# Kernel optimization log

Measured on AMD Instinct MI355X. Metric: run time of the kernel, lower is better.

The kernel has to match this reference:

```python
import jax, jax.numpy as jnp
import numpy as np

TAU = 100.0
DT = 20.0
ALPHA = DT / TAU  # 0.2, fixed buffer (train_alpha=False)


def setup_inputs() -> dict:
    key = jax.random.key(0)
    ks = jax.random.split(key, 12)
    T, B, I, H = 64, 32, 128, 256

    def lin(kw, out_f, in_f):
        bound = 1.0 / np.sqrt(in_f)
        kw1, kw2 = jax.random.split(kw)
        w = jax.random.uniform(kw1, (out_f, in_f), jnp.float32, -bound, bound)
        b = jax.random.uniform(kw2, (out_f,), jnp.float32, -bound, bound)
        return w, b

    w_i2h, b_i2h = lin(ks[0], H, I)
    w_h2h, b_h2h = lin(ks[1], H, H)
    w_i2c, b_i2c = lin(ks[2], H, I)
    w_c2c, b_c2c = lin(ks[3], H, H)
    w_c2t, b_c2t = lin(ks[4], H * H, H)
    x = jax.random.normal(ks[5], (T, B, I), jnp.float32)
    return {
        "input": x,
        "w_i2h": w_i2h, "b_i2h": b_i2h,
        "w_h2h": w_h2h, "b_h2h": b_h2h,
        "w_i2c": w_i2c, "b_i2c": b_i2c,
        "w_c2c": w_c2c, "b_c2c": b_c2c,
        "w_c2t": w_c2t, "b_c2t": b_c2t,
        "num_steps": 1,
    }


def reference(input, w_i2h, b_i2h, w_h2h, b_h2h, w_i2c, b_i2c,
              w_c2c, b_c2c, w_c2t, b_c2t, num_steps):
    H = w_i2h.shape[0]
    B = input.shape[1]
    a = jnp.float32(ALPHA)

    def recurrence(x, hidden, context):
        input_proj = x @ w_i2h.T + b_i2h                      # [B,H]
        tm = (context @ w_c2t.T + b_c2t).reshape(B, H, H)     # per-sample hypernet matrix
        transformed = jnp.einsum('bij,bj->bi', tm, input_proj)
        h_new = jax.nn.relu(context + transformed + hidden @ w_h2h.T + b_h2h)
        hidden = hidden * (1 - a) + h_new * a
        context_new = jax.nn.relu(context @ w_c2c.T + b_c2c + x @ w_i2c.T + b_i2c)
        context = context * (1 - a) + context_new * a
        hidden = transformed  # NOTE: faithful to source, overwrites leaky update
        return hidden, context

    def step(carry, x):
        hidden, context = carry
        for _ in range(num_steps):
            hidden, context = recurrence(x, hidden, context)
        return (hidden, context), hidden

    h0 = jnp.zeros((B, H), input.dtype)
    c0 = jnp.zeros((B, H), input.dtype)
    (hidden, context), output = jax.lax.scan(step, (h0, c0), input)
    return output, hidden, context
```

## Files before the change

kernel.cpp:

```cpp
#include <hip/hip_runtime.h>

#define TT 64
#define BB 32
#define II 128
#define HH 256
#define MM (TT*BB)

typedef __bf16  bf16x8  __attribute__((ext_vector_type(8)));
typedef float   f32x16  __attribute__((ext_vector_type(16)));
typedef _Float16 half2v __attribute__((ext_vector_type(2)));

__device__ __forceinline__ float bf2f(unsigned short u) {
    union { unsigned int i; float f; } v; v.i = ((unsigned int)u) << 16; return v.f;
}
__device__ __forceinline__ unsigned short f2bf(float f) {
    union { float f; unsigned int i; } v; v.f = f;
    unsigned int r = v.i + 0x7fffu + ((v.i >> 16) & 1u);
    return (unsigned short)(r >> 16);
}

struct F8 { float v[8]; };
__device__ __forceinline__ F8 load8(const void* base, int idx, int isf32) {
    F8 r;
    if (isf32) {
        const float4* p = (const float4*)((const float*)base + idx);
        float4 a = p[0], b = p[1];
        r.v[0]=a.x; r.v[1]=a.y; r.v[2]=a.z; r.v[3]=a.w;
        r.v[4]=b.x; r.v[5]=b.y; r.v[6]=b.z; r.v[7]=b.w;
    } else {
        uint4 u = *(const uint4*)((const unsigned short*)base + idx);
        const unsigned short* p = (const unsigned short*)&u;
#pragma unroll
        for (int j = 0; j < 8; ++j) r.v[j] = bf2f(p[j]);
    }
    return r;
}
__device__ __forceinline__ float load1(const void* base, int idx, int isf32) {
    return isf32 ? ((const float*)base)[idx]
                 : bf2f(((const unsigned short*)base)[idx]);
}

__device__ __forceinline__ float fdot2f(half2v a, half2v b, float c) {
#if __has_builtin(__builtin_amdgcn_fdot2)
    return __builtin_amdgcn_fdot2(a, b, c, false);
#else
    return c + (float)a.x*(float)b.x + (float)a.y*(float)b.y;
#endif
}

__global__ __launch_bounds__(256) void k0_sniff(
    const unsigned short* __restrict__ x, int* __restrict__ flag)
{
    __shared__ int cnt;
    if (threadIdx.x == 0) cnt = 0;
    __syncthreads();
    int c = 0;
    for (int i = threadIdx.x; i < 8192; i += 256) {
        unsigned int e = (x[i] >> 7) & 0xFFu;
        if (e >= 0xC0u) ++c;
    }
    atomicAdd(&cnt, c);
    __syncthreads();
    if (threadIdx.x == 0) flag[0] = (cnt > 16) ? 1 : 0;
}

__global__ __launch_bounds__(256) void k1_proj(
    const void* __restrict__ x,
    const void* __restrict__ w_i2h,
    const void* __restrict__ b_i2h,
    const void* __restrict__ w_i2c,
    const void* __restrict__ b_i2c,
    const int* __restrict__ flagp,
    unsigned short* __restrict__ ip,
    float* __restrict__ cin)
{
    const int isf32 = *flagp;
    const int tid = threadIdx.x;
    const int h = tid;
    const int mbase = blockIdx.x * 32;
    __shared__ __align__(16) _Float16 xs[32][II];

    half2v w1[II/2], w2[II/2];
#pragma unroll
    for (int c8 = 0; c8 < II/8; ++c8) {
        F8 f1 = load8(w_i2h, h*II + c8*8, isf32);
        F8 f2 = load8(w_i2c, h*II + c8*8, isf32);
#pragma unroll
        for (int j = 0; j < 4; ++j) {
            half2v a; a.x = (_Float16)f1.v[2*j]; a.y = (_Float16)f1.v[2*j+1];
            half2v b; b.x = (_Float16)f2.v[2*j]; b.y = (_Float16)f2.v[2*j+1];
            w1[c8*4 + j] = a;
            w2[c8*4 + j] = b;
        }
    }
    const float bb1 = load1(b_i2h, h, isf32);
    const float bb2 = load1(b_i2c, h, isf32);

    for (int u = tid; u < 32*II; u += 256)
        xs[u >> 7][u & (II-1)] = (_Float16)load1(x, (mbase + (u >> 7))*II + (u & (II-1)), isf32);
    __syncthreads();

    for (int mm = 0; mm < 32; ++mm) {
        const half2v* xv = (const half2v*)xs[mm];
        float a0=0,a1=0,a2=0,a3=0, c0=0,c1=0,c2=0,c3=0;
#pragma unroll
        for (int r = 0; r < II/2; r += 4) {
            half2v x0 = xv[r], x1 = xv[r+1], x2 = xv[r+2], x3 = xv[r+3];
            a0 = fdot2f(w1[r],   x0, a0);
            a1 = fdot2f(w1[r+1], x1, a1);
            a2 = fdot2f(w1[r+2], x2, a2);
            a3 = fdot2f(w1[r+3], x3, a3);
            c0 = fdot2f(w2[r],   x0, c0);
            c1 = fdot2f(w2[r+1], x1, c1);
            c2 = fdot2f(w2[r+2], x2, c2);
            c3 = fdot2f(w2[r+3], x3, c3);
        }
        ip[(mbase+mm)*HH + h]  = f2bf(((a0+a1)+(a2+a3)) + bb1);
        cin[(mbase+mm)*HH + h] = ((c0+c1)+(c2+c3)) + bb2;
    }
}

__global__ __launch_bounds__(256) void k2_ctx(
    const void* __restrict__ w_c2c,
    const void* __restrict__ b_c2c,
    const float* __restrict__ cin,
    const int* __restrict__ ns_ptr,
    const int* __restrict__ flagp,
    unsigned short* __restrict__ ctx_hist,
    void* __restrict__ out_base)
{
    const int isf32 = *flagp;
    const int b = blockIdx.x;
    const int h = threadIdx.x;
    const int ns = max(1, *ns_ptr);

    __shared__ __align__(16) _Float16 cs[2][HH];

    half2v w[HH/2];
#pragma unroll
    for (int c8 = 0; c8 < HH/8; ++c8) {
        F8 f = load8(w_c2c, h*HH + c8*8, isf32);
#pragma unroll
        for (int j = 0; j < 4; ++j) {
            half2v hv;
            hv.x = (_Float16)f.v[2*j];
            hv.y = (_Float16)f.v[2*j+1];
            w[c8*4 + j] = hv;
        }
    }
    const float bcc = load1(b_c2c, h, isf32);
    float ctxv = 0.0f;
    cs[0][h] = (_Float16)0.0f;
    __syncthreads();
    int cur = 0;

    for (int t = 0; t < TT; ++t) {
        const float cinv = cin[(t*BB + b)*HH + h];
        for (int s = 0; s < ns; ++s) {
            if (s == ns-1) ctx_hist[(t*BB + b)*HH + h] = f2bf(ctxv);
            float p0=0,p1=0,p2=0,p3=0;
            const float4* cp4 = (const float4*)cs[cur];
#pragma unroll
            for (int r4 = 0; r4 < HH/8; ++r4) {
                float4 blob = cp4[r4];
                const half2v* c2 = (const half2v*)&blob;
                p0 = fdot2f(w[r4*4+0], c2[0], p0);
                p1 = fdot2f(w[r4*4+1], c2[1], p1);
                p2 = fdot2f(w[r4*4+2], c2[2], p2);
                p3 = fdot2f(w[r4*4+3], c2[3], p3);
            }
            float cnew = fmaxf(((p0+p1)+(p2+p3)) + bcc + cinv, 0.0f);
            ctxv = 0.8f*ctxv + 0.2f*cnew;
            cs[cur^1][h] = (_Float16)ctxv;
            cur ^= 1;
            __syncthreads();
        }
    }
    const int cofs = MM*HH + BB*HH + b*HH + h;
    if (isf32) ((float*)out_base)[cofs] = ctxv;
    else       ((unsigned short*)out_base)[cofs] = f2bf(ctxv);
}

__global__ __launch_bounds__(512, 2) void k3_main(
    const unsigned short* __restrict__ ctx_hist,
    const void* __restrict__ wc,
    const void* __restrict__ bc,
    const unsigned short* __restrict__ ip,
    const int* __restrict__ flagp,
    void* __restrict__ out)
{
    extern __shared__ __align__(16) unsigned char lds[];
    unsigned short* Bs = (unsigned short*)lds;
    unsigned short* As = (unsigned short*)(lds + 131072);
    float*          TMf = (float*)(lds + 131072);

    const int isf32 = *flagp;
    const int tid  = threadIdx.x;
    const int lane = tid & 63;
    const int wave = tid >> 6;
    const int i    = blockIdx.x;
    const int mh   = wave & 3;
    const int jh   = wave >> 2;
    const int l31  = lane & 31;
    const int lhi  = lane >> 5;

    const int eml = tid >> 4;
    const int ecs = tid & 15;

    float bcp[16];
    {
        F8 f0 = load8(bc, i*HH + ecs*16,     isf32);
        F8 f1 = load8(bc, i*HH + ecs*16 + 8, isf32);
#pragma unroll
        for (int j = 0; j < 8; ++j) { bcp[j] = f0.v[j]; bcp[8+j] = f1.v[j]; }
    }

#pragma unroll
    for (int p = 0; p < 16; ++p) {
        int u = tid + p*512;
        int row = u >> 5, cu = u & 31;
        F8 f = load8(wc, (i*HH + row)*HH + cu*8, isf32);
        unsigned short tmp[8];
#pragma unroll
        for (int j = 0; j < 8; ++j) tmp[j] = f2bf(f.v[j]);
        *(uint4*)(Bs + row*256 + ((cu ^ (row & 7)) << 3)) = *(const uint4*)tmp;
    }

    for (int mc = 0; mc < 8; ++mc) {
        const int m0 = mc * 256;

        f32x16 acc[2][4];
#pragma unroll
        for (int a = 0; a < 2; ++a)
#pragma unroll
            for (int n = 0; n < 4; ++n)
#pragma unroll
                for (int r = 0; r < 16; ++r) acc[a][n][r] = 0.0f;

#pragma unroll
        for (int kc = 0; kc < 4; ++kc) {
            const int k0 = kc * 64;
#pragma unroll
            for (int p = 0; p < 4; ++p) {
                int u = tid + p*512;
                int row = u >> 3, cu = u & 7;
                uint4 v = *(const uint4*)(ctx_hist + (m0 + row)*HH + k0 + cu*8);
                *(uint4*)(As + row*64 + ((cu ^ (row & 7)) << 3)) = v;
            }
            __syncthreads();
#pragma unroll
            for (int ks = 0; ks < 4; ++ks) {
                const int cA = ks*2 + lhi;
                const int ra0 = mh*64 + l31;
                const int ra1 = ra0 + 32;
                bf16x8 a0 = *(const bf16x8*)(As + ra0*64 + ((cA ^ (ra0 & 7)) << 3));
                bf16x8 a1 = *(const bf16x8*)(As + ra1*64 + ((cA ^ (ra1 & 7)) << 3));
                const int cB = kc*8 + ks*2 + lhi;
                const int rb0 = jh*128 +       l31;
                const int rb1 = jh*128 + 32  + l31;
                const int rb2 = jh*128 + 64  + l31;
                const int rb3 = jh*128 + 96  + l31;
                bf16x8 b0 = *(const bf16x8*)(Bs + rb0*256 + ((cB ^ (rb0 & 7)) << 3));
                bf16x8 b1 = *(const bf16x8*)(Bs + rb1*256 + ((cB ^ (rb1 & 7)) << 3));
                bf16x8 b2 = *(const bf16x8*)(Bs + rb2*256 + ((cB ^ (rb2 & 7)) << 3));
                bf16x8 b3 = *(const bf16x8*)(Bs + rb3*256 + ((cB ^ (rb3 & 7)) << 3));
                acc[0][0] = __builtin_amdgcn_mfma_f32_32x32x16_bf16(a0, b0, acc[0][0], 0, 0, 0);
                acc[0][1] = __builtin_amdgcn_mfma_f32_32x32x16_bf16(a0, b1, acc[0][1], 0, 0, 0);
                acc[0][2] = __builtin_amdgcn_mfma_f32_32x32x16_bf16(a0, b2, acc[0][2], 0, 0, 0);
                acc[0][3] = __builtin_amdgcn_mfma_f32_32x32x16_bf16(a0, b3, acc[0][3], 0, 0, 0);
                acc[1][0] = __builtin_amdgcn_mfma_f32_32x32x16_bf16(a1, b0, acc[1][0], 0, 0, 0);
                acc[1][1] = __builtin_amdgcn_mfma_f32_32x32x16_bf16(a1, b1, acc[1][1], 0, 0, 0);
                acc[1][2] = __builtin_amdgcn_mfma_f32_32x32x16_bf16(a1, b2, acc[1][2], 0, 0, 0);
                acc[1][3] = __builtin_amdgcn_mfma_f32_32x32x16_bf16(a1, b3, acc[1][3], 0, 0, 0);
            }
            __syncthreads();
        }

#pragma unroll
        for (int ch = 0; ch < 8; ++ch) {
            if (mh == (ch >> 1)) {
                const int a = ch & 1;
#pragma unroll
                for (int n = 0; n < 4; ++n) {
                    const int j  = jh*128 + n*32 + l31;
                    const int ju = j >> 2, jo = j & 3;
#pragma unroll
                    for (int r = 0; r < 16; ++r) {
                        const int row16 = (r & 3) + 8*(r >> 2) + 4*lhi;
                        TMf[row16*256 + ((ju ^ (row16 & 7)) << 2) + jo] = acc[a][n][r];
                    }
                }
            }
            __syncthreads();
            {
                const int g = m0 + ch*32 + eml;
                float ipf[16];
                {
                    uint4 u0 = *(const uint4*)(ip + g*HH + ecs*16);
                    uint4 u1 = *(const uint4*)(ip + g*HH + ecs*16 + 8);
                    const unsigned short* p0 = (const unsigned short*)&u0;
                    const unsigned short* p1 = (const unsigned short*)&u1;
#pragma unroll
                    for (int j = 0; j < 8; ++j) { ipf[j] = bf2f(p0[j]); ipf[8+j] = bf2f(p1[j]); }
                }
                const float4* TM4 = (const float4*)TMf;
                float s = 0.0f;
#pragma unroll
                for (int u = 0; u < 4; ++u) {
                    float4 t = TM4[eml*64 + ((ecs*4 + u) ^ (eml & 7))];
                    s = fmaf(t.x + bcp[u*4+0], ipf[u*4+0], s);
                    s = fmaf(t.y + bcp[u*4+1], ipf[u*4+1], s);
                    s = fmaf(t.z + bcp[u*4+2], ipf[u*4+2], s);
                    s = fmaf(t.w + bcp[u*4+3], ipf[u*4+3], s);
                }
                s += __shfl_xor(s, 1);
                s += __shfl_xor(s, 2);
                s += __shfl_xor(s, 4);
                s += __shfl_xor(s, 8);
                if (ecs == 0) {
                    if (isf32) {
                        float* o = (float*)out;
                        o[g*HH + i] = s;
                        if (g >= MM - BB) o[MM*HH + (g - (MM-BB))*HH + i] = s;
                    } else {
                        unsigned short* o = (unsigned short*)out;
                        const unsigned short v = f2bf(s);
                        o[g*HH + i] = v;
                        if (g >= MM - BB) o[MM*HH + (g - (MM-BB))*HH + i] = v;
                    }
                }
            }
            __syncthreads();
        }
    }
}

extern "C" void kernel_launch(void* const* d_in, const int* in_sizes, int n_in,
                              void* d_out, int out_size, void* d_ws, size_t ws_size,
                              hipStream_t stream) {
    const void* x     = d_in[0];
    const void* w_i2h = d_in[1];
    const void* b_i2h = d_in[2];
    const void* w_i2c = d_in[5];
    const void* b_i2c = d_in[6];
    const void* w_c2c = d_in[7];
    const void* b_c2c = d_in[8];
    const void* w_c2t = d_in[9];
    const void* b_c2t = d_in[10];
    const int* ns     = (const int*)d_in[11];

    unsigned short* ip  = (unsigned short*)d_ws;
    unsigned short* ch  = (unsigned short*)((char*)d_ws + (size_t)MM*HH*2);
    float* cin          = (float*)((char*)d_ws + (size_t)MM*HH*4);
    int* flag           = (int*)((char*)d_ws + (size_t)MM*HH*8);

    static bool attr_done = false;
    (void)hipFuncSetAttribute((const void*)k3_main,
                              hipFuncAttributeMaxDynamicSharedMemorySize, 163840);
    (void)attr_done;

    k0_sniff<<<1, 256, 0, stream>>>((const unsigned short*)x, flag);
    k1_proj<<<64, 256, 0, stream>>>(x, w_i2h, b_i2h, w_i2c, b_i2c, flag, ip, cin);
    k2_ctx<<<BB, 256, 0, stream>>>(w_c2c, b_c2c, cin, ns, flag, ch, d_out);
    k3_main<<<256, 512, 163840, stream>>>(ch, w_c2t, b_c2t, ip, flag, d_out);
}
```

Measured before the change: 341.5 us.

## Prefetch A tiles into registers and reduce epilogue directly from MFMA accumulators

The main hypernet GEMM kernel now prefetches the next context-history tile into registers while the current tile is consumed by MFMAs. The epilogue drops the staged LDS round-trip of the transformed matrix and instead dots accumulators with the input projection in registers, reducing with shuffles. Results go to a transposed fp32 scratch buffer that a new transpose kernel writes out coalesced. This adds an extra launch and scratch traffic, and lowers launch bounds to one block per CU.

Result: slower. 405.6 us (+18.8%).

```diff
diff --git a/kernel.cpp b/kernel.cpp
--- a/kernel.cpp
+++ b/kernel.cpp
@@ -181,18 +181,18 @@
     else       ((unsigned short*)out_base)[cofs] = f2bf(ctxv);
 }
 
-__global__ __launch_bounds__(512, 2) void k3_main(
+__global__ __launch_bounds__(512, 1) void k3_main(
     const unsigned short* __restrict__ ctx_hist,
     const void* __restrict__ wc,
     const void* __restrict__ bc,
     const unsigned short* __restrict__ ip,
     const int* __restrict__ flagp,
-    void* __restrict__ out)
+    float* __restrict__ outT)
 {
     extern __shared__ __align__(16) unsigned char lds[];
     unsigned short* Bs = (unsigned short*)lds;
     unsigned short* As = (unsigned short*)(lds + 131072);
-    float*          TMf = (float*)(lds + 131072);
+    float*          part = (float*)(lds + 131072);
 
     const int isf32 = *flagp;
     const int tid  = threadIdx.x;
@@ -204,16 +204,10 @@
     const int l31  = lane & 31;
     const int lhi  = lane >> 5;
 
-    const int eml = tid >> 4;
-    const int ecs = tid & 15;
-
-    float bcp[16];
-    {
-        F8 f0 = load8(bc, i*HH + ecs*16,     isf32);
-        F8 f1 = load8(bc, i*HH + ecs*16 + 8, isf32);
-#pragma unroll
-        for (int j = 0; j < 8; ++j) { bcp[j] = f0.v[j]; bcp[8+j] = f1.v[j]; }
-    }
+    float bcv[4];
+#pragma unroll
+    for (int n = 0; n < 4; ++n)
+        bcv[n] = load1(bc, i*HH + jh*128 + n*32 + l31, isf32);
 
 #pragma unroll
     for (int p = 0; p < 16; ++p) {
@@ -226,6 +220,14 @@
         *(uint4*)(Bs + row*256 + ((cu ^ (row & 7)) << 3)) = *(const uint4*)tmp;
     }
 
+    uint4 areg[4];
+#pragma unroll
+    for (int p = 0; p < 4; ++p) {
+        int u = tid + p*512;
+        int row = u >> 3, cu = u & 7;
+        areg[p] = *(const uint4*)(ctx_hist + row*HH + cu*8);
+    }
+
     for (int mc = 0; mc < 8; ++mc) {
         const int m0 = mc * 256;
 
@@ -239,15 +241,27 @@
 
 #pragma unroll
         for (int kc = 0; kc < 4; ++kc) {
-            const int k0 = kc * 64;
+            __syncthreads();
 #pragma unroll
             for (int p = 0; p < 4; ++p) {
                 int u = tid + p*512;
                 int row = u >> 3, cu = u & 7;
-                uint4 v = *(const uint4*)(ctx_hist + (m0 + row)*HH + k0 + cu*8);
-                *(uint4*)(As + row*64 + ((cu ^ (row & 7)) << 3)) = v;
+                *(uint4*)(As + row*64 + ((cu ^ (row & 7)) << 3)) = areg[p];
             }
             __syncthreads();
+            {
+                int nmc = mc, nkc = kc + 1;
+                if (nkc == 4) { nkc = 0; nmc = mc + 1; }
+                if (nmc < 8) {
+                    const unsigned short* src = ctx_hist + (nmc*256)*HH + nkc*64;
+#pragma unroll
+                    for (int p = 0; p < 4; ++p) {
+                        int u = tid + p*512;
+                        int row = u >> 3, cu = u & 7;
+                        areg[p] = *(const uint4*)(src + row*HH + cu*8);
+                    }
+                }
+            }
 #pragma unroll
             for (int ks = 0; ks < 4; ++ks) {
                 const int cA = ks*2 + lhi;
@@ -273,64 +287,64 @@
                 acc[1][2] = __builtin_amdgcn_mfma_f32_32x32x16_bf16(a1, b2, acc[1][2], 0, 0, 0);
                 acc[1][3] = __builtin_amdgcn_mfma_f32_32x32x16_bf16(a1, b3, acc[1][3], 0, 0, 0);
             }
-            __syncthreads();
-        }
-
-#pragma unroll
-        for (int ch = 0; ch < 8; ++ch) {
-            if (mh == (ch >> 1)) {
-                const int a = ch & 1;
-#pragma unroll
-                for (int n = 0; n < 4; ++n) {
-                    const int j  = jh*128 + n*32 + l31;
-                    const int ju = j >> 2, jo = j & 3;
-#pragma unroll
-                    for (int r = 0; r < 16; ++r) {
-                        const int row16 = (r & 3) + 8*(r >> 2) + 4*lhi;
-                        TMf[row16*256 + ((ju ^ (row16 & 7)) << 2) + jo] = acc[a][n][r];
-                    }
-                }
-            }
-            __syncthreads();
-            {
-                const int g = m0 + ch*32 + eml;
-                float ipf[16];
-                {
-                    uint4 u0 = *(const uint4*)(ip + g*HH + ecs*16);
-                    uint4 u1 = *(const uint4*)(ip + g*HH + ecs*16 + 8);
-                    const unsigned short* p0 = (const unsigned short*)&u0;
-                    const unsigned short* p1 = (const unsigned short*)&u1;
-#pragma unroll
-                    for (int j = 0; j < 8; ++j) { ipf[j] = bf2f(p0[j]); ipf[8+j] = bf2f(p1[j]); }
-                }
-                const float4* TM4 = (const float4*)TMf;
-                float s = 0.0f;
-#pragma unroll
-                for (int u = 0; u < 4; ++u) {
-                    float4 t = TM4[eml*64 + ((ecs*4 + u) ^ (eml & 7))];
-                    s = fmaf(t.x + bcp[u*4+0], ipf[u*4+0], s);
-                    s = fmaf(t.y + bcp[u*4+1], ipf[u*4+1], s);
-                    s = fmaf(t.z + bcp[u*4+2], ipf[u*4+2], s);
-                    s = fmaf(t.w + bcp[u*4+3], ipf[u*4+3], s);
-                }
-                s += __shfl_xor(s, 1);
-                s += __shfl_xor(s, 2);
-                s += __shfl_xor(s, 4);
-                s += __shfl_xor(s, 8);
-                if (ecs == 0) {
-                    if (isf32) {
-                        float* o = (float*)out;
-                        o[g*HH + i] = s;
-                        if (g >= MM - BB) o[MM*HH + (g - (MM-BB))*HH + i] = s;
-                    } else {
-                        unsigned short* o = (unsigned short*)out;
-                        const unsigned short v = f2bf(s);
-                        o[g*HH + i] = v;
-                        if (g >= MM - BB) o[MM*HH + (g - (MM-BB))*HH + i] = v;
-                    }
-                }
-            }
-            __syncthreads();
+        }
+
+        __syncthreads();
+#pragma unroll
+        for (int a = 0; a < 2; ++a) {
+#pragma unroll
+            for (int r = 0; r < 16; ++r) {
+                const int rl = (r & 3) + 8*(r >> 2) + 4*lhi;
+                const int gm = m0 + mh*64 + a*32 + rl;
+                const unsigned short* ipr = ip + gm*HH + jh*128 + l31;
+                float p = 0.0f;
+#pragma unroll
+                for (int n = 0; n < 4; ++n)
+                    p = fmaf(acc[a][n][r] + bcv[n], bf2f(ipr[n*32]), p);
+                p += __shfl_xor(p, 1);
+                p += __shfl_xor(p, 2);
+                p += __shfl_xor(p, 4);
+                p += __shfl_xor(p, 8);
+                p += __shfl_xor(p, 16);
+                if (l31 == rl) part[jh*256 + mh*64 + a*32 + rl] = p;
+            }
+        }
+        __syncthreads();
+        if (tid < 256)
+            outT[(size_t)i*MM + m0 + tid] = part[tid] + part[256 + tid];
+    }
+}
+
+__global__ __launch_bounds__(256) void k4_tr(
+    const float* __restrict__ outT,
+    const int* __restrict__ flagp,
+    void* __restrict__ out)
+{
+    const int isf32 = *flagp;
+    __shared__ float tile[64][65];
+    const int m0 = blockIdx.x * 64, i0 = blockIdx.y * 64;
+    const int tm = threadIdx.x & 63, tq = threadIdx.x >> 6;
+#pragma unroll
+    for (int rep = 0; rep < 16; ++rep) {
+        int il = tq + rep*4;
+        tile[il][tm] = outT[(size_t)(i0 + il)*MM + m0 + tm];
+    }
+    __syncthreads();
+#pragma unroll
+    for (int rep = 0; rep < 16; ++rep) {
+        int ml = tq + rep*4;
+        int ii = tm;
+        float v = tile[ii][ml];
+        int mg = m0 + ml, ig = i0 + ii;
+        if (isf32) {
+            float* o = (float*)out;
+            o[(size_t)mg*HH + ig] = v;
+            if (mg >= MM - BB) o[(size_t)MM*HH + (mg - (MM-BB))*HH + ig] = v;
+        } else {
+            unsigned short* o = (unsigned short*)out;
+            unsigned short b = f2bf(v);
+            o[(size_t)mg*HH + ig] = b;
+            if (mg >= MM - BB) o[(size_t)MM*HH + (mg - (MM-BB))*HH + ig] = b;
         }
     }
 }
@@ -353,14 +367,14 @@
     unsigned short* ch  = (unsigned short*)((char*)d_ws + (size_t)MM*HH*2);
     float* cin          = (float*)((char*)d_ws + (size_t)MM*HH*4);
     int* flag           = (int*)((char*)d_ws + (size_t)MM*HH*8);
-
-    static bool attr_done = false;
+    float* outT         = (float*)((char*)d_ws + (size_t)MM*HH*8 + 1024);
+
     (void)hipFuncSetAttribute((const void*)k3_main,
                               hipFuncAttributeMaxDynamicSharedMemorySize, 163840);
-    (void)attr_done;
 
     k0_sniff<<<1, 256, 0, stream>>>((const unsigned short*)x, flag);
     k1_proj<<<64, 256, 0, stream>>>(x, w_i2h, b_i2h, w_i2c, b_i2c, flag, ip, cin);
     k2_ctx<<<BB, 256, 0, stream>>>(w_c2c, b_c2c, cin, ns, flag, ch, d_out);
-    k3_main<<<256, 512, 163840, stream>>>(ch, w_c2t, b_c2t, ip, flag, d_out);
-}
+    k3_main<<<256, 512, 163840, stream>>>(ch, w_c2t, b_c2t, ip, flag, outT);
+    k4_tr<<<dim3(32, 4), 256, 0, stream>>>(outT, flag, d_out);
+}
```
